# Performance work log

Hardware: AMD Instinct MI355X
Metric: run time of the kernel (lower is better)

The kernel has to match this reference:

```python
import jax, jax.numpy as jnp
import numpy as np

EPS = 1e-6

def _rmsnorm(x, w):
    rms = jax.lax.rsqrt(jnp.mean(x * x, axis=-1, keepdims=True) + EPS)
    return x * rms * w

def setup_inputs() -> dict:
    key = jax.random.key(0)
    ks = jax.random.split(key, 4)
    BS, N, D, DI = 4, 8192, 1024, 2048
    x = jax.random.normal(ks[0], (BS, N, D), dtype=jnp.float32)
    h_prev = jax.random.normal(ks[1], (BS, DI), dtype=jnp.float32)
    norm_w = jnp.ones((D,), dtype=jnp.float32)
    W_in = jax.random.normal(ks[2], (2 * DI, D), dtype=jnp.float32) * (1.0 / np.sqrt(D))
    b_in = jnp.zeros((2 * DI,), dtype=jnp.float32)
    W_out = jax.random.normal(ks[3], (D, DI), dtype=jnp.float32) * (1.0 / np.sqrt(DI))
    b_out = jnp.zeros((D,), dtype=jnp.float32)
    return {"x": x, "h_prev": h_prev, "norm_w": norm_w, "W_in": W_in,
            "b_in": b_in, "W_out": W_out, "b_out": b_out}

def _scan(a, b, h0):
    # h_t = a_t * h_{t-1} + b_t ; fold h0 into first step
    b = b.at[:, 0].set(a[:, 0] * h0 + b[:, 0])
    def combine(c1, c2):
        a1, b1 = c1
        a2, b2 = c2
        return (a2 * a1, a2 * b1 + b2)
    _, h = jax.lax.associative_scan(combine, (a, b), axis=1)
    return h  # [BS, N, E]

def reference(x, h_prev, norm_w, W_in, b_in, W_out, b_out):
    DI = W_out.shape[1]
    xn = _rmsnorm(x, norm_w)
    ab = jnp.einsum('bnd,ed->bne', xn, W_in) + b_in  # [BS, N, 2*DI]
    a_raw, b_raw = ab[..., :DI], ab[..., DI:]
    a = jax.nn.sigmoid(a_raw)
    b = jax.nn.silu(b_raw)
    h = _scan(a, b, h_prev)  # [BS, N, DI]
    out = jnp.einsum('bne,de->bnd', h, W_out) + b_out + x
    return out, h[:, -1]
```

## Files before the change

kernel.cpp:

```cpp
#include <hip/hip_runtime.h>
#include <stdint.h>
#include <stddef.h>

typedef __bf16 bf16;
typedef __attribute__((ext_vector_type(8))) __bf16 bf16x8;
typedef __attribute__((ext_vector_type(4))) __bf16 bf16x4;
typedef __attribute__((ext_vector_type(4))) float floatx4;

#define DEV static __device__ __forceinline__

DEV void async_load16(const void* g, void* l) {
  __builtin_amdgcn_global_load_lds(
      (__attribute__((address_space(1))) void*)(g),
      (__attribute__((address_space(3))) void*)(l),
      16, 0, 0);
}

DEV float bf16lo_to_f(uint32_t pv) {
  uint32_t b = pv << 16; float f; __builtin_memcpy(&f, &b, 4); return f;
}
DEV float bf16hi_to_f(uint32_t pv) {
  uint32_t b = pv & 0xffff0000u; float f; __builtin_memcpy(&f, &b, 4); return f;
}

__global__ __launch_bounds__(256)
void f2bf_kernel(const float* __restrict__ in, bf16* __restrict__ out, int n4)
{
  int i = blockIdx.x * 256 + threadIdx.x;
  if (i < n4) {
    float4 v = ((const float4*)in)[i];
    bf16x4 o = { (bf16)v.x, (bf16)v.y, (bf16)v.z, (bf16)v.w };
    ((bf16x4*)out)[i] = o;
  }
}

__global__ __launch_bounds__(256)
void rmsnorm_kernel(const float* __restrict__ x, const float* __restrict__ w,
                    bf16* __restrict__ xn)
{
  const int row = blockIdx.x;
  const int tid = threadIdx.x;
  float4 v = ((const float4*)(x + (size_t)row * 1024))[tid];
  float ss = v.x * v.x + v.y * v.y + v.z * v.z + v.w * v.w;
  #pragma unroll
  for (int off = 1; off < 64; off <<= 1)
    ss += __shfl_xor(ss, off, 64);
  __shared__ float red[4];
  if ((tid & 63) == 0) red[tid >> 6] = ss;
  __syncthreads();
  float tot = red[0] + red[1] + red[2] + red[3];
  float rms = rsqrtf(tot * (1.0f / 1024.0f) + 1e-6f);
  float4 wv = ((const float4*)w)[tid];
  bf16x4 o;
  o[0] = (bf16)(v.x * rms * wv.x);
  o[1] = (bf16)(v.y * rms * wv.y);
  o[2] = (bf16)(v.z * rms * wv.z);
  o[3] = (bf16)(v.w * rms * wv.w);
  ((bf16x4*)(xn + (size_t)row * 1024))[tid] = o;
}

template <int MODE>
__global__ __launch_bounds__(256)
void gemm_bt_kernel(const bf16* __restrict__ A, const bf16* __restrict__ B,
                    int N, int K, int numNt,
                    bf16* __restrict__ sb, float* __restrict__ out,
                    const float* __restrict__ bias,
                    const float* __restrict__ resid)
{
  __shared__ bf16 ldsA[128 * 64];
  __shared__ bf16 ldsB[128 * 64];

  const int GROUP_M = 16;
  int bid = blockIdx.x;
  int per_group = GROUP_M * numNt;
  int group = bid / per_group;
  int rem = bid - group * per_group;
  int mt = group * GROUP_M + (rem % GROUP_M);
  int nt = rem / GROUP_M;
  const int m0 = mt * 128, n0 = nt * 128;

  const int tid  = threadIdx.x;
  const int lane = tid & 63;
  const int wave = tid >> 6;
  const int wm   = (wave & 1) * 64;
  const int wn   = (wave >> 1) * 64;
  const int l15  = lane & 15;
  const int quad = lane >> 4;

  floatx4 acc[4][4];
  #pragma unroll
  for (int i = 0; i < 4; ++i)
    #pragma unroll
    for (int j = 0; j < 4; ++j)
      acc[i][j] = (floatx4){0.f, 0.f, 0.f, 0.f};

  for (int kt = 0; kt < K; kt += 64) {
    #pragma unroll
    for (int i = 0; i < 4; ++i) {
      int c   = tid + i * 256;
      int row = c >> 3;
      int kgg = (c & 7) ^ (row & 7);
      async_load16(A + (size_t)(m0 + row) * K + kt + kgg * 8, &ldsA[c * 8]);
      async_load16(B + (size_t)(n0 + row) * K + kt + kgg * 8, &ldsB[c * 8]);
    }
    __syncthreads();
    #pragma unroll
    for (int ks = 0; ks < 2; ++ks) {
      bf16x8 af[4], bfr[4];
      #pragma unroll
      for (int i = 0; i < 4; ++i) {
        int row = wm + i * 16 + l15;
        int kg  = ks * 4 + quad;
        af[i]  = *(const bf16x8*)&ldsA[(row * 8 + (kg ^ (row & 7))) * 8];
        int col = wn + i * 16 + l15;
        bfr[i] = *(const bf16x8*)&ldsB[(col * 8 + (kg ^ (col & 7))) * 8];
      }
      #pragma unroll
      for (int i = 0; i < 4; ++i)
        #pragma unroll
        for (int j = 0; j < 4; ++j)
          acc[i][j] = __builtin_amdgcn_mfma_f32_16x16x32_bf16(af[i], bfr[j], acc[i][j], 0, 0, 0);
    }
    __syncthreads();
  }

  #pragma unroll
  for (int i = 0; i < 4; ++i) {
    #pragma unroll
    for (int j = 0; j < 4; ++j) {
      #pragma unroll
      for (int r = 0; r < 4; ++r) {
        int row = m0 + wm + i * 16 + quad * 4 + r;
        int col = n0 + wn + j * 16 + l15;
        float v = acc[i][j][r];
        if (MODE == 1) {
          v += bias[col];
          if (col < 2048) {
            sb[((size_t)row * 2048 + col) * 2] = (bf16)(1.0f / (1.0f + __expf(v)));
          } else {
            sb[((size_t)row * 2048 + (col - 2048)) * 2 + 1] =
                (bf16)(v / (1.0f + __expf(-v)));
          }
        } else {
          v += bias[col] + resid[(size_t)row * N + col];
          out[(size_t)row * N + col] = v;
        }
      }
    }
  }
}

__global__ __launch_bounds__(256)
void scan_phase1(const uint32_t* __restrict__ sb,
                 float* __restrict__ Ac, float* __restrict__ Bc)
{
  int g = blockIdx.x * 256 + threadIdx.x;
  int e     = g & 2047;
  int chunk = (g >> 11) & 15;
  int seq   = g >> 15;
  size_t base = ((size_t)(seq * 8192 + chunk * 512)) * 2048 + e;
  float A = 1.0f, Bv = 0.0f;
  #pragma unroll 8
  for (int n = 0; n < 512; ++n) {
    uint32_t pv = sb[base + (size_t)n * 2048];
    float a = 1.0f - bf16lo_to_f(pv);
    float b = bf16hi_to_f(pv);
    A *= a;
    Bv = a * Bv + b;
  }
  Ac[g] = A;
  Bc[g] = Bv;
}

__global__ __launch_bounds__(256)
void scan_phase2(const float* __restrict__ Ac, const float* __restrict__ Bc,
                 const float* __restrict__ h_prev,
                 float* __restrict__ carry, float* __restrict__ h_last)
{
  int g = blockIdx.x * 256 + threadIdx.x;
  int e = g & 2047;
  int seq = g >> 11;
  float h = h_prev[g];
  #pragma unroll
  for (int c = 0; c < 16; ++c) {
    size_t idx = ((size_t)(seq * 16 + c)) * 2048 + e;
    carry[idx] = h;
    h = Ac[idx] * h + Bc[idx];
  }
  h_last[g] = h;
}

__global__ __launch_bounds__(256)
void scan_phase3(const uint32_t* __restrict__ sb,
                 const float* __restrict__ carry, bf16* __restrict__ h_out)
{
  int g = blockIdx.x * 256 + threadIdx.x;
  int e     = g & 2047;
  int chunk = (g >> 11) & 15;
  int seq   = g >> 15;
  float h = carry[((size_t)(seq * 16 + chunk)) * 2048 + e];
  size_t base = ((size_t)(seq * 8192 + chunk * 512)) * 2048 + e;
  #pragma unroll 8
  for (int n = 0; n < 512; ++n) {
    uint32_t pv = sb[base + (size_t)n * 2048];
    float a = 1.0f - bf16lo_to_f(pv);
    float b = bf16hi_to_f(pv);
    h = a * h + b;
    h_out[base + (size_t)n * 2048] = (bf16)h;
  }
}

extern "C" void kernel_launch(void* const* d_in, const int* in_sizes, int n_in,
                              void* d_out, int out_size, void* d_ws, size_t ws_size,
                              hipStream_t stream)
{
  const float* x      = (const float*)d_in[0];
  const float* h_prev = (const float*)d_in[1];
  const float* norm_w = (const float*)d_in[2];
  const float* W_in   = (const float*)d_in[3];
  const float* b_in   = (const float*)d_in[4];
  const float* W_out  = (const float*)d_in[5];
  const float* b_out  = (const float*)d_in[6];

  float* out    = (float*)d_out;
  float* h_last = out + (size_t)33554432;

  int BSl = 4, passes = 1;
  {
    size_t need4 = 14155776 + (size_t)4 * 8192 * 2048 * 4
                            + (size_t)4 * 8192 * 1024 * 2
                            + (size_t)4 * 8192 * 2048 * 2;
    if (ws_size < need4) { BSl = 1; passes = 4; }
  }
  const size_t Mrows = (size_t)BSl * 8192;
  char* ws = (char*)d_ws;
  bf16*  Win_b  = (bf16*)(ws);
  bf16*  Wout_b = (bf16*)(ws + 8388608);
  size_t acN    = (size_t)BSl * 16 * 2048;
  float* Ac     = (float*)(ws + 12582912);
  float* Bc     = (float*)(ws + 12582912 + acN * 4);
  float* carry  = (float*)(ws + 12582912 + acN * 8);
  char*  p0     = ws + 12582912 + acN * 12;
  bf16*  sb     = (bf16*)(p0);
  bf16*  xn     = (bf16*)(p0 + Mrows * 2048 * 4);
  bf16*  h_arr  = (bf16*)(p0 + Mrows * 2048 * 4 + Mrows * 1024 * 2);

  f2bf_kernel<<<4096, 256, 0, stream>>>(W_in, Win_b, 4194304 / 4);
  f2bf_kernel<<<2048, 256, 0, stream>>>(W_out, Wout_b, 2097152 / 4);

  for (int p = 0; p < passes; ++p) {
    const float* xp = x + (size_t)p * Mrows * 1024;

    rmsnorm_kernel<<<(int)Mrows, 256, 0, stream>>>(xp, norm_w, xn);

    int numMt = (int)(Mrows / 128);
    gemm_bt_kernel<1><<<numMt * 32, 256, 0, stream>>>(
        xn, Win_b, 4096, 1024, 32, sb, nullptr, b_in, nullptr);

    scan_phase1<<<BSl * 128, 256, 0, stream>>>((const uint32_t*)sb, Ac, Bc);
    scan_phase2<<<BSl * 8, 256, 0, stream>>>(Ac, Bc, h_prev + (size_t)p * BSl * 2048,
                                             carry, h_last + (size_t)p * BSl * 2048);
    scan_phase3<<<BSl * 128, 256, 0, stream>>>((const uint32_t*)sb, carry, h_arr);

    gemm_bt_kernel<2><<<numMt * 8, 256, 0, stream>>>(
        h_arr, Wout_b, 1024, 2048, 8, nullptr, out + (size_t)p * Mrows * 1024,
        b_out, xp);
  }
}
```

Measured before the change: 973.9 us.

## Interleave W_in rows so GEMM epilogue writes packed (a,b) words; double scan chunks

The rows of W_in and the bias are permuted so that each 32-column group of the first GEMM output holds 16 sigmoid-gate columns next to their 16 matching silu columns. The epilogue can then compute both values in registers and write one packed 32-bit word, instead of two scattered 16-bit stores. The scan now splits each sequence into 32 chunks of 256 instead of 16 of 512, doubling parallelism in phases 1 and 3. The costs are an extra permutation kernel for the weights and bias, more carry data, and a longer serial loop in phase 2.

```diff
diff --git a/kernel.cpp b/kernel.cpp
--- a/kernel.cpp
+++ b/kernel.cpp
@@ -23,6 +23,13 @@
   uint32_t b = pv & 0xffff0000u; float f; __builtin_memcpy(&f, &b, 4); return f;
 }
 
+DEV int win_orig_row(int c) {
+  int jt16 = c >> 4;
+  int is_b = jt16 & 1;
+  int p    = (jt16 >> 1) * 16 + (c & 15);
+  return p + is_b * 2048;
+}
+
 __global__ __launch_bounds__(256)
 void f2bf_kernel(const float* __restrict__ in, bf16* __restrict__ out, int n4)
 {
@@ -32,6 +39,23 @@
     bf16x4 o = { (bf16)v.x, (bf16)v.y, (bf16)v.z, (bf16)v.w };
     ((bf16x4*)out)[i] = o;
   }
+}
+
+__global__ __launch_bounds__(256)
+void f2bf_win_perm(const float* __restrict__ in, bf16* __restrict__ out)
+{
+  int c = blockIdx.x;
+  int orig = win_orig_row(c);
+  float4 v = ((const float4*)(in + (size_t)orig * 1024))[threadIdx.x];
+  bf16x4 o = { (bf16)v.x, (bf16)v.y, (bf16)v.z, (bf16)v.w };
+  ((bf16x4*)(out + (size_t)c * 1024))[threadIdx.x] = o;
+}
+
+__global__ __launch_bounds__(256)
+void bias_perm_kernel(const float* __restrict__ b_in, float* __restrict__ biasP)
+{
+  int c = blockIdx.x * 256 + threadIdx.x;
+  biasP[c] = b_in[win_orig_row(c)];
 }
 
 __global__ __launch_bounds__(256)
@@ -63,7 +87,7 @@
 __global__ __launch_bounds__(256)
 void gemm_bt_kernel(const bf16* __restrict__ A, const bf16* __restrict__ B,
                     int N, int K, int numNt,
-                    bf16* __restrict__ sb, float* __restrict__ out,
+                    uint32_t* __restrict__ sbw, float* __restrict__ out,
                     const float* __restrict__ bias,
                     const float* __restrict__ resid)
 {
@@ -124,25 +148,40 @@
     __syncthreads();
   }
 
-  #pragma unroll
-  for (int i = 0; i < 4; ++i) {
-    #pragma unroll
-    for (int j = 0; j < 4; ++j) {
+  if (MODE == 1) {
+    #pragma unroll
+    for (int i = 0; i < 4; ++i) {
       #pragma unroll
-      for (int r = 0; r < 4; ++r) {
-        int row = m0 + wm + i * 16 + quad * 4 + r;
-        int col = n0 + wn + j * 16 + l15;
-        float v = acc[i][j][r];
-        if (MODE == 1) {
-          v += bias[col];
-          if (col < 2048) {
-            sb[((size_t)row * 2048 + col) * 2] = (bf16)(1.0f / (1.0f + __expf(v)));
-          } else {
-            sb[((size_t)row * 2048 + (col - 2048)) * 2 + 1] =
-                (bf16)(v / (1.0f + __expf(-v)));
-          }
-        } else {
-          v += bias[col] + resid[(size_t)row * N + col];
+      for (int pair = 0; pair < 2; ++pair) {
+        int j0 = pair * 2;
+        float bs = bias[n0 + wn + j0 * 16 + l15];
+        float bb = bias[n0 + wn + j0 * 16 + 16 + l15];
+        int ch = (n0 >> 1) + (wn >> 1) + pair * 16 + l15;
+        #pragma unroll
+        for (int r = 0; r < 4; ++r) {
+          int row = m0 + wm + i * 16 + quad * 4 + r;
+          float vs = acc[i][j0][r] + bs;
+          float vb = acc[i][j0 + 1][r] + bb;
+          float s  = 1.0f / (1.0f + __expf(vs));
+          float sv = 1.0f / (1.0f + __expf(vb));
+          float bv = vb - vb * sv;
+          union { bf16 h[2]; uint32_t u; } pk;
+          pk.h[0] = (bf16)s;
+          pk.h[1] = (bf16)bv;
+          sbw[(size_t)row * 2048 + ch] = pk.u;
+        }
+      }
+    }
+  } else {
+    #pragma unroll
+    for (int i = 0; i < 4; ++i) {
+      #pragma unroll
+      for (int j = 0; j < 4; ++j) {
+        #pragma unroll
+        for (int r = 0; r < 4; ++r) {
+          int row = m0 + wm + i * 16 + quad * 4 + r;
+          int col = n0 + wn + j * 16 + l15;
+          float v = acc[i][j][r] + bias[col] + resid[(size_t)row * N + col];
           out[(size_t)row * N + col] = v;
         }
       }
@@ -156,12 +195,12 @@
 {
   int g = blockIdx.x * 256 + threadIdx.x;
   int e     = g & 2047;
-  int chunk = (g >> 11) & 15;
-  int seq   = g >> 15;
-  size_t base = ((size_t)(seq * 8192 + chunk * 512)) * 2048 + e;
+  int chunk = (g >> 11) & 31;
+  int seq   = g >> 16;
+  size_t base = ((size_t)(seq * 8192 + chunk * 256)) * 2048 + e;
   float A = 1.0f, Bv = 0.0f;
   #pragma unroll 8
-  for (int n = 0; n < 512; ++n) {
+  for (int n = 0; n < 256; ++n) {
     uint32_t pv = sb[base + (size_t)n * 2048];
     float a = 1.0f - bf16lo_to_f(pv);
     float b = bf16hi_to_f(pv);
@@ -182,8 +221,8 @@
   int seq = g >> 11;
   float h = h_prev[g];
   #pragma unroll
-  for (int c = 0; c < 16; ++c) {
-    size_t idx = ((size_t)(seq * 16 + c)) * 2048 + e;
+  for (int c = 0; c < 32; ++c) {
+    size_t idx = ((size_t)(seq * 32 + c)) * 2048 + e;
     carry[idx] = h;
     h = Ac[idx] * h + Bc[idx];
   }
@@ -196,12 +235,12 @@
 {
   int g = blockIdx.x * 256 + threadIdx.x;
   int e     = g & 2047;
-  int chunk = (g >> 11) & 15;
-  int seq   = g >> 15;
-  float h = carry[((size_t)(seq * 16 + chunk)) * 2048 + e];
-  size_t base = ((size_t)(seq * 8192 + chunk * 512)) * 2048 + e;
+  int chunk = (g >> 11) & 31;
+  int seq   = g >> 16;
+  float h = carry[((size_t)(seq * 32 + chunk)) * 2048 + e];
+  size_t base = ((size_t)(seq * 8192 + chunk * 256)) * 2048 + e;
   #pragma unroll 8
-  for (int n = 0; n < 512; ++n) {
+  for (int n = 0; n < 256; ++n) {
     uint32_t pv = sb[base + (size_t)n * 2048];
     float a = 1.0f - bf16lo_to_f(pv);
     float b = bf16hi_to_f(pv);
@@ -227,26 +266,31 @@
 
   int BSl = 4, passes = 1;
   {
-    size_t need4 = 14155776 + (size_t)4 * 8192 * 2048 * 4
-                            + (size_t)4 * 8192 * 1024 * 2
-                            + (size_t)4 * 8192 * 2048 * 2;
+    size_t need4 = 8388608 + 4194304 + 16384
+                 + 3 * ((size_t)4 * 32 * 2048 * 4)
+                 + (size_t)4 * 8192 * 2048 * 4
+                 + (size_t)4 * 8192 * 1024 * 2
+                 + (size_t)4 * 8192 * 2048 * 2;
     if (ws_size < need4) { BSl = 1; passes = 4; }
   }
   const size_t Mrows = (size_t)BSl * 8192;
   char* ws = (char*)d_ws;
   bf16*  Win_b  = (bf16*)(ws);
   bf16*  Wout_b = (bf16*)(ws + 8388608);
-  size_t acN    = (size_t)BSl * 16 * 2048;
-  float* Ac     = (float*)(ws + 12582912);
-  float* Bc     = (float*)(ws + 12582912 + acN * 4);
-  float* carry  = (float*)(ws + 12582912 + acN * 8);
-  char*  p0     = ws + 12582912 + acN * 12;
-  bf16*  sb     = (bf16*)(p0);
+  float* biasP  = (float*)(ws + 12582912);
+  size_t acN    = (size_t)BSl * 32 * 2048;
+  char*  pa     = ws + 12599296;
+  float* Ac     = (float*)(pa);
+  float* Bc     = (float*)(pa + acN * 4);
+  float* carry  = (float*)(pa + acN * 8);
+  char*  p0     = pa + acN * 12;
+  uint32_t* sbw = (uint32_t*)(p0);
   bf16*  xn     = (bf16*)(p0 + Mrows * 2048 * 4);
   bf16*  h_arr  = (bf16*)(p0 + Mrows * 2048 * 4 + Mrows * 1024 * 2);
 
-  f2bf_kernel<<<4096, 256, 0, stream>>>(W_in, Win_b, 4194304 / 4);
+  f2bf_win_perm<<<4096, 256, 0, stream>>>(W_in, Win_b);
   f2bf_kernel<<<2048, 256, 0, stream>>>(W_out, Wout_b, 2097152 / 4);
+  bias_perm_kernel<<<16, 256, 0, stream>>>(b_in, biasP);
 
   for (int p = 0; p < passes; ++p) {
     const float* xp = x + (size_t)p * Mrows * 1024;
@@ -255,12 +299,12 @@
 
     int numMt = (int)(Mrows / 128);
     gemm_bt_kernel<1><<<numMt * 32, 256, 0, stream>>>(
-        xn, Win_b, 4096, 1024, 32, sb, nullptr, b_in, nullptr);
-
-    scan_phase1<<<BSl * 128, 256, 0, stream>>>((const uint32_t*)sb, Ac, Bc);
+        xn, Win_b, 4096, 1024, 32, sbw, nullptr, biasP, nullptr);
+
+    scan_phase1<<<BSl * 256, 256, 0, stream>>>(sbw, Ac, Bc);
     scan_phase2<<<BSl * 8, 256, 0, stream>>>(Ac, Bc, h_prev + (size_t)p * BSl * 2048,
                                              carry, h_last + (size_t)p * BSl * 2048);
-    scan_phase3<<<BSl * 128, 256, 0, stream>>>((const uint32_t*)sb, carry, h_arr);
+    scan_phase3<<<BSl * 256, 256, 0, stream>>>(sbw, carry, h_arr);
 
     gemm_bt_kernel<2><<<numMt * 8, 256, 0, stream>>>(
         h_arr, Wout_b, 1024, 2048, 8, nullptr, out + (size_t)p * Mrows * 1024,
```

After: 965.4 us. No clear change (-0.9%).
